# Performance work log

Hardware: AMD Instinct MI355X
Metric: run time of the kernel (lower is better)

## Reference

```python
import jax, jax.numpy as jnp
import numpy as np

B_, N_, D_ = 2, 2048, 512
E_ = 2 * D_          # d_inner = expand * dim
S_ = 16              # d_state
K_ = 4               # d_conv
R_ = 32              # dt_rank = ceil(dim/16)
C_ = 512             # cond_dim


def setup_inputs() -> dict:
    key = jax.random.key(0)
    ks = jax.random.split(key, 12)
    r = lambda i, sh, s=0.02: jax.random.normal(ks[i], sh, dtype=jnp.float32) * s
    return {
        "x": jax.random.normal(ks[0], (B_, N_, D_), dtype=jnp.float32),
        "cond": jax.random.normal(ks[1], (B_, C_), dtype=jnp.float32),
        "ln_g": jnp.ones((D_,), jnp.float32),
        "ln_b": jnp.zeros((D_,), jnp.float32),
        "W_in": r(2, (D_, 2 * E_)),            # in_proj (no bias)
        "conv_w": r(3, (E_, K_), 0.1),          # depthwise causal conv
        "conv_b": jnp.zeros((E_,), jnp.float32),
        "W_x": r(4, (E_, R_ + 2 * S_)),         # x_proj -> dt,B,C
        "W_dt": r(5, (R_, E_), 0.1),
        "b_dt": jnp.full((E_,), -4.6, jnp.float32),  # softplus(-4.6)~0.01
        "A_log": jnp.log(jnp.broadcast_to(jnp.arange(1, S_ + 1, dtype=jnp.float32), (E_, S_))),
        "D_skip": jnp.ones((E_,), jnp.float32),
        "W_out": r(6, (E_, D_)),                # out_proj (no bias)
        "film_gw": r(7, (C_, D_)),
        "film_gb": jnp.ones((D_,), jnp.float32),
        "film_bw": r(8, (C_, D_)),
        "film_bb": jnp.zeros((D_,), jnp.float32),
    }


def reference(x, cond, ln_g, ln_b, W_in, conv_w, conv_b, W_x, W_dt, b_dt,
              A_log, D_skip, W_out, film_gw, film_gb, film_bw, film_bb):
    # --- LayerNorm ---
    mu = x.mean(-1, keepdims=True)
    var = ((x - mu) ** 2).mean(-1, keepdims=True)
    xn = (x - mu) * jax.lax.rsqrt(var + 1e-5) * ln_g + ln_b

    # --- Mamba ---
    xz = xn @ W_in                                  # [B,N,2E]
    u, z = jnp.split(xz, 2, axis=-1)                # [B,N,E] each
    # causal depthwise conv1d (kernel K_), unrolled over small K
    up = jnp.pad(u, ((0, 0), (K_ - 1, 0), (0, 0)))
    uc = conv_b + sum(up[:, k:k + N_, :] * conv_w[:, k] for k in range(K_))
    uc = jax.nn.silu(uc)                            # [B,N,E]

    x_dbl = uc @ W_x                                # [B,N,R+2S]
    dt, Bm, Cm = jnp.split(x_dbl, [R_, R_ + S_], axis=-1)
    delta = jax.nn.softplus(dt @ W_dt + b_dt)       # [B,N,E]

    A = -jnp.exp(A_log)                             # [E,S]
    dA = jnp.exp(delta[..., None] * A)              # [B,N,E,S]
    dBu = (delta * uc)[..., None] * Bm[:, :, None, :]  # [B,N,E,S]

    def step(h, ins):
        dA_t, dBu_t, C_t = ins                      # [B,E,S],[B,E,S],[B,S]
        h = dA_t * h + dBu_t
        y = jnp.einsum('bes,bs->be', h, C_t)
        return h, y

    h0 = jnp.zeros((x.shape[0], E_, S_), dtype=x.dtype)
    _, ys = jax.lax.scan(step, h0,
                         (dA.swapaxes(0, 1), dBu.swapaxes(0, 1), Cm.swapaxes(0, 1)))
    y = ys.swapaxes(0, 1) + D_skip * uc             # [B,N,E]
    y = y * jax.nn.silu(z)
    out = y @ W_out                                 # [B,N,D]

    # --- FiLM ---
    gamma = cond @ film_gw + film_gb                # [B,D]
    beta = cond @ film_bw + film_bb
    return gamma[:, None, :] * out + beta[:, None, :]
```

## Files before the change

kernel.cpp:

```cpp
#include <hip/hip_runtime.h>
#include <hip/hip_bf16.h>
#include <math.h>

#define B_ 2
#define N_ 2048
#define D_ 512
#define E_ 1024
#define S_ 16
#define R_ 32
#define C_ 512
#define CH_ 32
#define NC_ (N_ / CH_)

using short8 = __attribute__((ext_vector_type(8))) short;
using f32x4  = __attribute__((ext_vector_type(4))) float;
using f32x16 = __attribute__((ext_vector_type(16))) float;

__device__ __forceinline__ short f2bf(float f) {
    union { float f; unsigned u; } x; x.f = f;
    unsigned r = (x.u + 0x7fffu + ((x.u >> 16) & 1u)) >> 16;
    return (short)r;
}
__device__ __forceinline__ float bf2f(short s) {
    union { unsigned u; float f; } x;
    x.u = ((unsigned)(unsigned short)s) << 16;
    return x.f;
}
__device__ __forceinline__ void gl_lds16(const void* g, void* l) {
    __builtin_amdgcn_global_load_lds((const __attribute__((address_space(1))) void*)g,
                                     (__attribute__((address_space(3))) void*)l, 16, 0, 0);
}

__global__ __launch_bounds__(256) void prep_kernel(
    const float* __restrict__ x, short* __restrict__ xnb,
    const float* __restrict__ W_in, short* __restrict__ Wint,
    const float* __restrict__ W_out, short* __restrict__ Woutt,
    const float* __restrict__ W_x, short* __restrict__ Wxt,
    const float* __restrict__ W_dt, short* __restrict__ Wdtt,
    const float* __restrict__ cond,
    const float* __restrict__ lng, const float* __restrict__ lnb,
    const float* __restrict__ gw, const float* __restrict__ gb,
    const float* __restrict__ bw, const float* __restrict__ bb,
    float* __restrict__ gamma, float* __restrict__ beta) {
    __shared__ __align__(16) float smem[2112];
    int bid = blockIdx.x;
    int tid = threadIdx.x;
    if (bid < 8) {
        float* cs = smem;
        float* red = smem + 1024;
        int d0 = bid * 64;
#pragma unroll
        for (int i = tid; i < 2 * C_ / 4; i += 256) {
            int b = i >> 7;
            int c4 = (i & 127) * 4;
            *(float4*)&cs[b * C_ + c4] = *(const float4*)(cond + (size_t)b * C_ + c4);
        }
        __syncthreads();
        int dl = tid & 63, ks = tid >> 6;
        int d = d0 + dl;
        float g0 = 0.f, g1 = 0.f, bt0 = 0.f, bt1 = 0.f;
#pragma unroll 4
        for (int k = ks * 128; k < ks * 128 + 128; k++) {
            float wg = gw[(size_t)k * D_ + d];
            float wb = bw[(size_t)k * D_ + d];
            float c0 = cs[k], c1 = cs[C_ + k];
            g0 = fmaf(c0, wg, g0);
            g1 = fmaf(c1, wg, g1);
            bt0 = fmaf(c0, wb, bt0);
            bt1 = fmaf(c1, wb, bt1);
        }
        red[(ks * 64 + dl) * 4 + 0] = g0; red[(ks * 64 + dl) * 4 + 1] = g1;
        red[(ks * 64 + dl) * 4 + 2] = bt0; red[(ks * 64 + dl) * 4 + 3] = bt1;
        __syncthreads();
        if (ks == 0) {
            float s0 = 0.f, s1 = 0.f, s2 = 0.f, s3 = 0.f;
#pragma unroll
            for (int q = 0; q < 4; q++) {
                s0 += red[(q * 64 + dl) * 4 + 0]; s1 += red[(q * 64 + dl) * 4 + 1];
                s2 += red[(q * 64 + dl) * 4 + 2]; s3 += red[(q * 64 + dl) * 4 + 3];
            }
            float gbv = gb[d], bbv = bb[d];
            gamma[d] = s0 + gbv;
            gamma[D_ + d] = s1 + gbv;
            beta[d] = s2 + bbv;
            beta[D_ + d] = s3 + bbv;
        }
    } else if (bid < 1640) {
        const float* W; short* Wt; int K, N, bx, by;
        int r = bid - 8;
        if (r < 1024)      { W = W_in;  Wt = Wint;  K = 512;  N = 2048; bx = r % 64; by = r / 64; }
        else if (r < 1536) { r -= 1024; W = W_out; Wt = Woutt; K = 1024; N = 512; bx = r % 16; by = r / 16; }
        else if (r < 1600) { r -= 1536; W = W_x;   Wt = Wxt;   K = 1024; N = 64;  bx = r % 2;  by = r / 2; }
        else               { r -= 1600; W = W_dt;  Wt = Wdtt;  K = 32;   N = 1024; bx = r;     by = 0; }
        float (*t)[33] = (float(*)[33])smem;
        int n0 = bx * 32, k0 = by * 32;
        int c = tid & 31, rr0 = tid >> 5;
#pragma unroll
        for (int rr = rr0; rr < 32; rr += 8)
            t[rr][c] = W[(size_t)(k0 + rr) * N + n0 + c];
        __syncthreads();
#pragma unroll
        for (int rr = rr0; rr < 32; rr += 8)
            Wt[(size_t)(n0 + rr) * K + k0 + c] = f2bf(t[c][rr]);
    } else {
        int t = bid - 1640;
        float2 v = *(const float2*)(x + (size_t)t * D_ + tid * 2);
        float s = v.x + v.y;
        float s2 = fmaf(v.x, v.x, v.y * v.y);
#pragma unroll
        for (int o = 32; o >= 1; o >>= 1) {
            s += __shfl_down(s, o);
            s2 += __shfl_down(s2, o);
        }
        int wid = tid >> 6;
        if ((tid & 63) == 0) { smem[wid] = s; smem[4 + wid] = s2; }
        __syncthreads();
        if (tid == 0) {
            float sum = smem[0] + smem[1] + smem[2] + smem[3];
            float sum2 = smem[4] + smem[5] + smem[6] + smem[7];
            float mu = sum * (1.f / (float)D_);
            float var = sum2 * (1.f / (float)D_) - mu * mu;
            smem[8] = mu;
            smem[9] = rsqrtf(var + 1e-5f);
        }
        __syncthreads();
        float mu = smem[8], rs = smem[9];
        float2 gv = *(const float2*)(lng + tid * 2);
        float2 bv = *(const float2*)(lnb + tid * 2);
        short2 o;
        o.x = f2bf((v.x - mu) * rs * gv.x + bv.x);
        o.y = f2bf((v.y - mu) * rs * gv.y + bv.y);
        *(short2*)(xnb + (size_t)t * D_ + tid * 2) = o;
    }
}

template <int BM, int BN, bool FILM, bool OBF>
__global__ __launch_bounds__(256) void gemm_bf16(
    const short* __restrict__ A, const short* __restrict__ Bt, void* __restrict__ Cv,
    int M, int N, int K,
    const float* __restrict__ gamma, const float* __restrict__ beta) {
    constexpr int BK = 64;
    constexpr int WM = BM / 2, WN = BN / 2;
    constexpr int MR = WM / 32, NR = WN / 32;
    __shared__ __align__(16) short As[BM * BK];
    __shared__ __align__(16) short Bs[BN * BK];
    int tid = threadIdx.x;
    int lane = tid & 63, w = tid >> 6;
    int wr = w >> 1, wc = w & 1;
    int lid = blockIdx.x;
    int chunk = gridDim.x >> 3;
    int swz = (lid & 7) * chunk + (lid >> 3);
    int ntiles = N / BN;
    int m0 = (swz / ntiles) * BM, n0 = (swz % ntiles) * BN;
    int lr = lane >> 3, lc = lane & 7;

    f32x16 acc[MR][NR];
#pragma unroll
    for (int i = 0; i < MR; i++)
#pragma unroll
        for (int j = 0; j < NR; j++)
#pragma unroll
            for (int r = 0; r < 16; r++) acc[i][j][r] = 0.f;

    int l31 = lane & 31, hk = (lane >> 5) * 8;

    for (int k0 = 0; k0 < K; k0 += BK) {
        __syncthreads();
#pragma unroll
        for (int ch = w; ch < BM / 8; ch += 4)
            gl_lds16(&A[(size_t)(m0 + ch * 8 + lr) * K + k0 + lc * 8], &As[ch * 512]);
#pragma unroll
        for (int ch = w; ch < BN / 8; ch += 4)
            gl_lds16(&Bt[(size_t)(n0 + ch * 8 + lr) * K + k0 + lc * 8], &Bs[ch * 512]);
        __syncthreads();
#pragma unroll
        for (int kk = 0; kk < 4; kk++) {
            short8 a[MR], b[NR];
#pragma unroll
            for (int i = 0; i < MR; i++)
                a[i] = *(const short8*)&As[(wr * WM + i * 32 + l31) * BK + kk * 16 + hk];
#pragma unroll
            for (int j = 0; j < NR; j++)
                b[j] = *(const short8*)&Bs[(wc * WN + j * 32 + l31) * BK + kk * 16 + hk];
#pragma unroll
            for (int i = 0; i < MR; i++)
#pragma unroll
                for (int j = 0; j < NR; j++)
                    acc[i][j] = __builtin_amdgcn_mfma_f32_32x32x16_bf16(a[i], b[j], acc[i][j], 0, 0, 0);
        }
    }
    int rbase = 4 * (lane >> 5);
    int bi = m0 >> 11;
#pragma unroll
    for (int i = 0; i < MR; i++)
#pragma unroll
        for (int j = 0; j < NR; j++) {
            int col = n0 + wc * WN + j * 32 + l31;
            float gm = 1.f, bt = 0.f;
            if (FILM) {
                gm = gamma[bi * D_ + col];
                bt = beta[bi * D_ + col];
            }
#pragma unroll
            for (int r = 0; r < 16; r++) {
                int row = m0 + wr * WM + i * 32 + rbase + (r & 3) + 8 * (r >> 2);
                float v = acc[i][j][r];
                if (FILM) v = gm * v + bt;
                if constexpr (OBF)
                    ((short*)Cv)[(size_t)row * N + col] = f2bf(v);
                else
                    ((float*)Cv)[(size_t)row * N + col] = v;
            }
        }
}

__global__ __launch_bounds__(512) void mid_kernel(
    const short* __restrict__ xzb, const float* __restrict__ cw, const float* __restrict__ cb,
    const short* __restrict__ Wxt,
    const short* __restrict__ Wdtt,
    const float* __restrict__ bdt,
    short* __restrict__ ucb, float* __restrict__ xdbl, short* __restrict__ deltab) {
    constexpr int LDU = 1032;
    __shared__ __align__(16) short u[16 * LDU];
    __shared__ __align__(16) float xd2[2][16 * 68];
    int tid = threadIdx.x;
    int t0 = blockIdx.x * 16;
    int n0 = t0 & (N_ - 1);
    {
        int c8 = (tid & 127) * 8;
        int base = (tid >> 7) * 4;
        float4 wv[8];
        float cbv[8];
#pragma unroll
        for (int j = 0; j < 8; j++) {
            wv[j] = *(const float4*)(cw + (c8 + j) * 4);
            cbv[j] = cb[c8 + j];
        }
        float uf[7][8];
#pragma unroll
        for (int j = 0; j < 7; j++) {
            short8 v = {0, 0, 0, 0, 0, 0, 0, 0};
            if (n0 + base - 3 + j >= 0)
                v = *(const short8*)&xzb[(size_t)(t0 + base - 3 + j) * (2 * E_) + c8];
#pragma unroll
            for (int q = 0; q < 8; q++) uf[j][q] = bf2f(v[q]);
        }
#pragma unroll
        for (int k = 0; k < 4; k++) {
            int n = base + k;
            short8 o;
#pragma unroll
            for (int q = 0; q < 8; q++) {
                float a = fmaf(wv[q].x, uf[k][q],
                          fmaf(wv[q].y, uf[k + 1][q],
                          fmaf(wv[q].z, uf[k + 2][q],
                          fmaf(wv[q].w, uf[k + 3][q], cbv[q]))));
                float v = a / (1.f + __expf(-a));
                o[q] = f2bf(v);
            }
            *(short8*)&ucb[(size_t)(t0 + n) * E_ + c8] = o;
            *(short8*)&u[n * LDU + c8] = o;
        }
    }
    __syncthreads();
    int lane = tid & 63, w = tid >> 6;
    int cg = w & 3, kh = w >> 2;
    int l15 = lane & 15, kq = (lane >> 4) * 8;
    f32x4 acc4 = {0.f, 0.f, 0.f, 0.f};
#pragma unroll 8
    for (int k0 = 0; k0 < 16; k0++) {
        int kk = kh * 512 + k0 * 32;
        short8 af = *(const short8*)&u[l15 * LDU + kk + kq];
        short8 bfr = *(const short8*)&Wxt[(size_t)(cg * 16 + l15) * E_ + kk + kq];
        acc4 = __builtin_amdgcn_mfma_f32_16x16x32_bf16(af, bfr, acc4, 0, 0, 0);
    }
#pragma unroll
    for (int j = 0; j < 4; j++)
        xd2[kh][((lane >> 4) * 4 + j) * 68 + cg * 16 + l15] = acc4[j];
    __syncthreads();
    if (tid < 256) {
        int r = tid >> 4, c4 = (tid & 15) * 4;
        float4 a = *(const float4*)&xd2[0][r * 68 + c4];
        float4 b = *(const float4*)&xd2[1][r * 68 + c4];
        a.x += b.x; a.y += b.y; a.z += b.z; a.w += b.w;
        *(float4*)&xd2[0][r * 68 + c4] = a;
        *(float4*)&xdbl[(size_t)(t0 + r) * 64 + c4] = a;
    }
    __syncthreads();
    float av[8];
    *(float4*)&av[0] = *(const float4*)&xd2[0][l15 * 68 + kq];
    *(float4*)&av[4] = *(const float4*)&xd2[0][l15 * 68 + kq + 4];
    short8 ab;
#pragma unroll
    for (int j = 0; j < 8; j++) ab[j] = f2bf(av[j]);
    int row4 = (lane >> 4) * 4;
#pragma unroll 4
    for (int t = 0; t < 8; t++) {
        int e = w * 128 + t * 16 + l15;
        short8 bb = *(const short8*)&Wdtt[(size_t)e * 32 + kq];
        f32x4 c4v = {0.f, 0.f, 0.f, 0.f};
        c4v = __builtin_amdgcn_mfma_f32_16x16x32_bf16(ab, bb, c4v, 0, 0, 0);
        float bv = bdt[e];
#pragma unroll
        for (int j = 0; j < 4; j++) {
            float xv = c4v[j] + bv;
            float sp = (xv > 20.f) ? xv : log1pf(__expf(xv));
            deltab[(size_t)(t0 + row4 + j) * E_ + e] = f2bf(sp);
        }
    }
}

__global__ __launch_bounds__(256) void scan_p1(const short* __restrict__ deltab,
                                               const short* __restrict__ ucb,
                                               const float* __restrict__ xdbl,
                                               const float* __restrict__ A_log,
                                               float* __restrict__ hend,
                                               float* __restrict__ cumd) {
    int blk = blockIdx.x;
    int eq = blk & 3;
    int c = (blk >> 2) & (NC_ - 1);
    int b = blk >> 8;
    int tid = threadIdx.x;
    int e = eq * 256 + tid;
    __shared__ float Bsl[CH_][16];
    int base = (b * N_ + c * CH_) * 64;
    for (int i = tid; i < CH_ * 16; i += 256) {
        int n = i >> 4, col = i & 15;
        Bsl[n][col] = xdbl[base + n * 64 + R_ + col];
    }
    float Aes[16];
    const float4* al = (const float4*)(A_log + e * 16);
#pragma unroll
    for (int j = 0; j < 4; j++) {
        float4 a = al[j];
        Aes[j * 4 + 0] = -__expf(a.x);
        Aes[j * 4 + 1] = -__expf(a.y);
        Aes[j * 4 + 2] = -__expf(a.z);
        Aes[j * 4 + 3] = -__expf(a.w);
    }
    __syncthreads();
    float h[16];
#pragma unroll
    for (int s = 0; s < 16; s++) h[s] = 0.f;
    float cum = 0.f;
    const short* dp = deltab + (size_t)(b * N_ + c * CH_) * E_ + e;
    const short* up = ucb + (size_t)(b * N_ + c * CH_) * E_ + e;
#pragma unroll 2
    for (int n = 0; n < CH_; n++) {
        float dv = bf2f(dp[n * E_]);
        float uv = bf2f(up[n * E_]);
        float du = dv * uv;
        cum += dv;
        float Bl[16];
#pragma unroll
        for (int j = 0; j < 4; j++) *(float4*)&Bl[j * 4] = *(const float4*)&Bsl[n][j * 4];
#pragma unroll
        for (int s = 0; s < 16; s++) {
            float dA = __expf(dv * Aes[s]);
            h[s] = fmaf(dA, h[s], du * Bl[s]);
        }
    }
    size_t ob = (size_t)(b * NC_ + c) * 16 * E_ + e;
#pragma unroll
    for (int s = 0; s < 16; s++) hend[ob + (size_t)s * E_] = h[s];
    cumd[(size_t)(b * NC_ + c) * E_ + e] = cum;
}

__global__ __launch_bounds__(256) void scan_comb(float* __restrict__ hend,
                                                 const float* __restrict__ cumd,
                                                 const float* __restrict__ A_log) {
    __shared__ float lh[64][65];
    __shared__ float lp[64][65];
    int blk = blockIdx.x;
    int et = blk & 15;
    int s = (blk >> 4) & 15;
    int b = blk >> 8;
    int e0 = et * 64;
    int tid = threadIdx.x;
    int lane = tid & 63, w = tid >> 6;
    for (int i = tid; i < 64 * 64; i += 256) {
        int c = i >> 6, e = i & 63;
        lh[c][e] = hend[((size_t)((b * NC_ + c) * 16) + s) * E_ + e0 + e];
        lp[c][e] = cumd[(size_t)(b * NC_ + c) * E_ + e0 + e];
    }
    __syncthreads();
#pragma unroll 4
    for (int q = 0; q < 16; q++) {
        int e = w * 16 + q;
        float Aes = -__expf(A_log[(e0 + e) * 16 + s]);
        float A = __expf(Aes * lp[lane][e]);
        float Bv = lh[lane][e];
#pragma unroll
        for (int off = 1; off < 64; off <<= 1) {
            float Ap = __shfl_up(A, off);
            float Bp = __shfl_up(Bv, off);
            if (lane >= off) {
                Bv = fmaf(A, Bp, Bv);
                A *= Ap;
            }
        }
        float hB = __shfl_up(Bv, 1);
        lh[lane][e] = (lane == 0) ? 0.f : hB;
    }
    __syncthreads();
    for (int i = tid; i < 64 * 64; i += 256) {
        int c = i >> 6, e = i & 63;
        hend[((size_t)((b * NC_ + c) * 16) + s) * E_ + e0 + e] = lh[c][e];
    }
}

__global__ __launch_bounds__(256) void scan_p3(const short* __restrict__ deltab,
                                               const short* __restrict__ ucb,
                                               const float* __restrict__ xdbl,
                                               const short* __restrict__ xzb,
                                               const float* __restrict__ A_log,
                                               const float* __restrict__ D_skip,
                                               const float* __restrict__ hend,
                                               short* __restrict__ yb) {
    int blk = blockIdx.x;
    int eq = blk & 3;
    int c = (blk >> 2) & (NC_ - 1);
    int b = blk >> 8;
    int tid = threadIdx.x;
    int e = eq * 256 + tid;
    __shared__ float Bsl[CH_][16];
    __shared__ float Csl[CH_][16];
    int base = (b * N_ + c * CH_) * 64;
    for (int i = tid; i < CH_ * 32; i += 256) {
        int n = i >> 5, col = i & 31;
        float v = xdbl[base + n * 64 + R_ + col];
        if (col < 16) Bsl[n][col] = v;
        else Csl[n][col - 16] = v;
    }
    float Aes[16];
    const float4* al = (const float4*)(A_log + e * 16);
#pragma unroll
    for (int j = 0; j < 4; j++) {
        float4 a = al[j];
        Aes[j * 4 + 0] = -__expf(a.x);
        Aes[j * 4 + 1] = -__expf(a.y);
        Aes[j * 4 + 2] = -__expf(a.z);
        Aes[j * 4 + 3] = -__expf(a.w);
    }
    float dsk = D_skip[e];
    float h[16];
    size_t ob = (size_t)(b * NC_ + c) * 16 * E_ + e;
#pragma unroll
    for (int s = 0; s < 16; s++) h[s] = hend[ob + (size_t)s * E_];
    __syncthreads();
    const short* dp = deltab + (size_t)(b * N_ + c * CH_) * E_ + e;
    const short* up = ucb + (size_t)(b * N_ + c * CH_) * E_ + e;
    const short* zp = xzb + (size_t)(b * N_ + c * CH_) * (2 * E_) + E_ + e;
    short* yp = yb + (size_t)(b * N_ + c * CH_) * E_ + e;
#pragma unroll 2
    for (int n = 0; n < CH_; n++) {
        float dv = bf2f(dp[n * E_]);
        float uv = bf2f(up[n * E_]);
        float du = dv * uv;
        float Bl[16], Cl[16];
#pragma unroll
        for (int j = 0; j < 4; j++) {
            *(float4*)&Bl[j * 4] = *(const float4*)&Bsl[n][j * 4];
            *(float4*)&Cl[j * 4] = *(const float4*)&Csl[n][j * 4];
        }
        float y = 0.f;
#pragma unroll
        for (int s = 0; s < 16; s++) {
            float dA = __expf(dv * Aes[s]);
            h[s] = fmaf(dA, h[s], du * Bl[s]);
            y = fmaf(h[s], Cl[s], y);
        }
        float zv = bf2f(zp[n * 2 * E_]);
        float yy = y + dsk * uv;
        yy = yy * (zv / (1.f + __expf(-zv)));
        yp[n * E_] = f2bf(yy);
    }
}

extern "C" void kernel_launch(void* const* d_in, const int* in_sizes, int n_in,
                              void* d_out, int out_size, void* d_ws, size_t ws_size,
                              hipStream_t stream) {
    const float* x       = (const float*)d_in[0];
    const float* cond    = (const float*)d_in[1];
    const float* ln_g    = (const float*)d_in[2];
    const float* ln_b    = (const float*)d_in[3];
    const float* W_in    = (const float*)d_in[4];
    const float* conv_w  = (const float*)d_in[5];
    const float* conv_b  = (const float*)d_in[6];
    const float* W_x     = (const float*)d_in[7];
    const float* W_dt    = (const float*)d_in[8];
    const float* b_dt    = (const float*)d_in[9];
    const float* A_log   = (const float*)d_in[10];
    const float* D_skip  = (const float*)d_in[11];
    const float* W_out   = (const float*)d_in[12];
    const float* film_gw = (const float*)d_in[13];
    const float* film_gb = (const float*)d_in[14];
    const float* film_bw = (const float*)d_in[15];
    const float* film_bb = (const float*)d_in[16];
    float* out = (float*)d_out;

    float* ws = (float*)d_ws;
    float* xdbl  = ws;
    float* gamma = xdbl + 262144;
    float* beta  = gamma + 1024;
    float* hend  = beta + 1024;
    float* cumd  = hend + 2097152;
    short* xzb   = (short*)(cumd + 131072);
    short* ucb   = xzb + 8388608;
    short* deltab = ucb + 4194304;
    short* Wint  = deltab + 4194304;
    short* Woutt = Wint + 1048576;
    short* yb    = Woutt + 524288;
    short* Wxt   = yb + 4194304;
    short* Wdtt  = Wxt + 65536;
    short* xnb   = Wdtt + 32768;

    prep_kernel<<<5736, 256, 0, stream>>>(
        x, xnb, W_in, Wint, W_out, Woutt, W_x, Wxt, W_dt, Wdtt,
        cond, ln_g, ln_b, film_gw, film_gb, film_bw, film_bb, gamma, beta);

    gemm_bf16<128, 128, false, true>
        <<<512, 256, 0, stream>>>(
            xnb, Wint, xzb, B_ * N_, 2 * E_, D_, nullptr, nullptr);

    mid_kernel<<<B_ * N_ / 16, 512, 0, stream>>>(
        xzb, conv_w, conv_b, Wxt, Wdtt, b_dt, ucb, xdbl, deltab);

    scan_p1<<<B_ * NC_ * 4, 256, 0, stream>>>(deltab, ucb, xdbl, A_log, hend, cumd);
    scan_comb<<<B_ * S_ * (E_ / 64), 256, 0, stream>>>(hend, cumd, A_log);
    scan_p3<<<B_ * NC_ * 4, 256, 0, stream>>>(deltab, ucb, xdbl, xzb, A_log, D_skip, hend, yb);

    gemm_bf16<64, 64, true, false>
        <<<512, 256, 0, stream>>>(
            yb, Woutt, out, B_ * N_, D_, E_, gamma, beta);
}
```

Measured before the change: 136.8 us.

## Overlap weight prep with first GEMM and store scan carry states in bf16

```diff
diff --git a/kernel.cpp b/kernel.cpp
--- a/kernel.cpp
+++ b/kernel.cpp
@@ -31,24 +31,136 @@
                                      (__attribute__((address_space(3))) void*)l, 16, 0, 0);
 }
 
-__global__ __launch_bounds__(256) void prep_kernel(
+__device__ __forceinline__ void transpose32(const float* __restrict__ W, short* __restrict__ Wt,
+                                            int K, int N, int bx, int by, float (*t)[33], int tid) {
+    int n0 = bx * 32, k0 = by * 32;
+    int c = tid & 31, rr0 = tid >> 5;
+#pragma unroll
+    for (int rr = rr0; rr < 32; rr += 8)
+        t[rr][c] = W[(size_t)(k0 + rr) * N + n0 + c];
+    __syncthreads();
+#pragma unroll
+    for (int rr = rr0; rr < 32; rr += 8)
+        Wt[(size_t)(n0 + rr) * K + k0 + c] = f2bf(t[c][rr]);
+}
+
+__global__ __launch_bounds__(256) void prep1_kernel(
     const float* __restrict__ x, short* __restrict__ xnb,
-    const float* __restrict__ W_in, short* __restrict__ Wint,
+    const float* __restrict__ lng, const float* __restrict__ lnb,
+    const float* __restrict__ W_in, short* __restrict__ Wint) {
+    __shared__ __align__(16) float smem[32 * 33];
+    int bid = blockIdx.x;
+    int tid = threadIdx.x;
+    if (bid < 1024) {
+        int t = bid * 4 + (tid >> 6);
+        int lane = tid & 63;
+        const float* src = x + (size_t)t * D_ + lane * 8;
+        float4 v0 = *(const float4*)src;
+        float4 v1 = *(const float4*)(src + 4);
+        float s = v0.x + v0.y + v0.z + v0.w + v1.x + v1.y + v1.z + v1.w;
+        float s2 = v0.x * v0.x;
+        s2 = fmaf(v0.y, v0.y, s2); s2 = fmaf(v0.z, v0.z, s2); s2 = fmaf(v0.w, v0.w, s2);
+        s2 = fmaf(v1.x, v1.x, s2); s2 = fmaf(v1.y, v1.y, s2);
+        s2 = fmaf(v1.z, v1.z, s2); s2 = fmaf(v1.w, v1.w, s2);
+#pragma unroll
+        for (int o = 32; o >= 1; o >>= 1) {
+            s += __shfl_xor(s, o);
+            s2 += __shfl_xor(s2, o);
+        }
+        float mu = s * (1.f / (float)D_);
+        float var = s2 * (1.f / (float)D_) - mu * mu;
+        float rs = rsqrtf(var + 1e-5f);
+        float4 g0 = *(const float4*)(lng + lane * 8);
+        float4 g1 = *(const float4*)(lng + lane * 8 + 4);
+        float4 b0 = *(const float4*)(lnb + lane * 8);
+        float4 b1 = *(const float4*)(lnb + lane * 8 + 4);
+        short8 o;
+        o[0] = f2bf((v0.x - mu) * rs * g0.x + b0.x);
+        o[1] = f2bf((v0.y - mu) * rs * g0.y + b0.y);
+        o[2] = f2bf((v0.z - mu) * rs * g0.z + b0.z);
+        o[3] = f2bf((v0.w - mu) * rs * g0.w + b0.w);
+        o[4] = f2bf((v1.x - mu) * rs * g1.x + b1.x);
+        o[5] = f2bf((v1.y - mu) * rs * g1.y + b1.y);
+        o[6] = f2bf((v1.z - mu) * rs * g1.z + b1.z);
+        o[7] = f2bf((v1.w - mu) * rs * g1.w + b1.w);
+        *(short8*)(xnb + (size_t)t * D_ + lane * 8) = o;
+    } else {
+        int r = bid - 1024;
+        transpose32(W_in, Wint, 512, 2048, r % 64, r / 64, (float(*)[33])smem, tid);
+    }
+}
+
+__global__ __launch_bounds__(256) void gemm1_hybrid(
+    const short* __restrict__ A, const short* __restrict__ Bt, short* __restrict__ Cb,
     const float* __restrict__ W_out, short* __restrict__ Woutt,
     const float* __restrict__ W_x, short* __restrict__ Wxt,
     const float* __restrict__ W_dt, short* __restrict__ Wdtt,
     const float* __restrict__ cond,
-    const float* __restrict__ lng, const float* __restrict__ lnb,
     const float* __restrict__ gw, const float* __restrict__ gb,
     const float* __restrict__ bw, const float* __restrict__ bb,
     float* __restrict__ gamma, float* __restrict__ beta) {
-    __shared__ __align__(16) float smem[2112];
+    __shared__ __align__(16) char smem[32768];
     int bid = blockIdx.x;
     int tid = threadIdx.x;
-    if (bid < 8) {
-        float* cs = smem;
-        float* red = smem + 1024;
-        int d0 = bid * 64;
+    if (bid < 512) {
+        constexpr int BM = 128, BN = 128, BK = 64;
+        constexpr int M = 4096, N = 2048, K = 512;
+        short* As = (short*)smem;
+        short* Bs = As + BM * BK;
+        int lane = tid & 63, w = tid >> 6;
+        int wr = w >> 1, wc = w & 1;
+        int swz = (bid & 7) * 64 + (bid >> 3);
+        int m0 = (swz >> 4) * BM, n0 = (swz & 15) * BN;
+        int lr = lane >> 3, lc = lane & 7;
+        f32x16 acc[2][2];
+#pragma unroll
+        for (int i = 0; i < 2; i++)
+#pragma unroll
+            for (int j = 0; j < 2; j++)
+#pragma unroll
+                for (int r = 0; r < 16; r++) acc[i][j][r] = 0.f;
+        int l31 = lane & 31, hk = (lane >> 5) * 8;
+        for (int k0 = 0; k0 < K; k0 += BK) {
+            __syncthreads();
+#pragma unroll
+            for (int ch = w; ch < BM / 8; ch += 4)
+                gl_lds16(&A[(size_t)(m0 + ch * 8 + lr) * K + k0 + lc * 8], &As[ch * 512]);
+#pragma unroll
+            for (int ch = w; ch < BN / 8; ch += 4)
+                gl_lds16(&Bt[(size_t)(n0 + ch * 8 + lr) * K + k0 + lc * 8], &Bs[ch * 512]);
+            __syncthreads();
+#pragma unroll
+            for (int kk = 0; kk < 4; kk++) {
+                short8 a[2], b[2];
+#pragma unroll
+                for (int i = 0; i < 2; i++)
+                    a[i] = *(const short8*)&As[(wr * 64 + i * 32 + l31) * BK + kk * 16 + hk];
+#pragma unroll
+                for (int j = 0; j < 2; j++)
+                    b[j] = *(const short8*)&Bs[(wc * 64 + j * 32 + l31) * BK + kk * 16 + hk];
+#pragma unroll
+                for (int i = 0; i < 2; i++)
+#pragma unroll
+                    for (int j = 0; j < 2; j++)
+                        acc[i][j] = __builtin_amdgcn_mfma_f32_32x32x16_bf16(a[i], b[j], acc[i][j], 0, 0, 0);
+            }
+        }
+        int rbase = 4 * (lane >> 5);
+#pragma unroll
+        for (int i = 0; i < 2; i++)
+#pragma unroll
+            for (int j = 0; j < 2; j++) {
+                int col = n0 + wc * 64 + j * 32 + l31;
+#pragma unroll
+                for (int r = 0; r < 16; r++) {
+                    int row = m0 + wr * 64 + i * 32 + rbase + (r & 3) + 8 * (r >> 2);
+                    Cb[(size_t)row * N + col] = f2bf(acc[i][j][r]);
+                }
+            }
+    } else if (bid < 520) {
+        float* cs = (float*)smem;
+        float* red = (float*)smem + 1024;
+        int d0 = (bid - 512) * 64;
 #pragma unroll
         for (int i = tid; i < 2 * C_ / 4; i += 256) {
             int b = i >> 7;
@@ -85,58 +197,21 @@
             beta[d] = s2 + bbv;
             beta[D_ + d] = s3 + bbv;
         }
-    } else if (bid < 1640) {
-        const float* W; short* Wt; int K, N, bx, by;
-        int r = bid - 8;
-        if (r < 1024)      { W = W_in;  Wt = Wint;  K = 512;  N = 2048; bx = r % 64; by = r / 64; }
-        else if (r < 1536) { r -= 1024; W = W_out; Wt = Woutt; K = 1024; N = 512; bx = r % 16; by = r / 16; }
-        else if (r < 1600) { r -= 1536; W = W_x;   Wt = Wxt;   K = 1024; N = 64;  bx = r % 2;  by = r / 2; }
-        else               { r -= 1600; W = W_dt;  Wt = Wdtt;  K = 32;   N = 1024; bx = r;     by = 0; }
-        float (*t)[33] = (float(*)[33])smem;
-        int n0 = bx * 32, k0 = by * 32;
-        int c = tid & 31, rr0 = tid >> 5;
-#pragma unroll
-        for (int rr = rr0; rr < 32; rr += 8)
-            t[rr][c] = W[(size_t)(k0 + rr) * N + n0 + c];
-        __syncthreads();
-#pragma unroll
-        for (int rr = rr0; rr < 32; rr += 8)
-            Wt[(size_t)(n0 + rr) * K + k0 + c] = f2bf(t[c][rr]);
+    } else if (bid < 1032) {
+        int r = bid - 520;
+        transpose32(W_out, Woutt, 1024, 512, r % 16, r / 16, (float(*)[33])smem, tid);
+    } else if (bid < 1096) {
+        int r = bid - 1032;
+        transpose32(W_x, Wxt, 1024, 64, r % 2, r / 2, (float(*)[33])smem, tid);
     } else {
-        int t = bid - 1640;
-        float2 v = *(const float2*)(x + (size_t)t * D_ + tid * 2);
-        float s = v.x + v.y;
-        float s2 = fmaf(v.x, v.x, v.y * v.y);
-#pragma unroll
-        for (int o = 32; o >= 1; o >>= 1) {
-            s += __shfl_down(s, o);
-            s2 += __shfl_down(s2, o);
-        }
-        int wid = tid >> 6;
-        if ((tid & 63) == 0) { smem[wid] = s; smem[4 + wid] = s2; }
-        __syncthreads();
-        if (tid == 0) {
-            float sum = smem[0] + smem[1] + smem[2] + smem[3];
-            float sum2 = smem[4] + smem[5] + smem[6] + smem[7];
-            float mu = sum * (1.f / (float)D_);
-            float var = sum2 * (1.f / (float)D_) - mu * mu;
-            smem[8] = mu;
-            smem[9] = rsqrtf(var + 1e-5f);
-        }
-        __syncthreads();
-        float mu = smem[8], rs = smem[9];
-        float2 gv = *(const float2*)(lng + tid * 2);
-        float2 bv = *(const float2*)(lnb + tid * 2);
-        short2 o;
-        o.x = f2bf((v.x - mu) * rs * gv.x + bv.x);
-        o.y = f2bf((v.y - mu) * rs * gv.y + bv.y);
-        *(short2*)(xnb + (size_t)t * D_ + tid * 2) = o;
-    }
-}
-
-template <int BM, int BN, bool FILM, bool OBF>
-__global__ __launch_bounds__(256) void gemm_bf16(
-    const short* __restrict__ A, const short* __restrict__ Bt, void* __restrict__ Cv,
+        int r = bid - 1096;
+        transpose32(W_dt, Wdtt, 32, 1024, r, 0, (float(*)[33])smem, tid);
+    }
+}
+
+template <int BM, int BN>
+__global__ __launch_bounds__(256) void gemm2_kernel(
+    const short* __restrict__ A, const short* __restrict__ Bt, float* __restrict__ Cf,
     int M, int N, int K,
     const float* __restrict__ gamma, const float* __restrict__ beta) {
     constexpr int BK = 64;
@@ -196,20 +271,12 @@
 #pragma unroll
         for (int j = 0; j < NR; j++) {
             int col = n0 + wc * WN + j * 32 + l31;
-            float gm = 1.f, bt = 0.f;
-            if (FILM) {
-                gm = gamma[bi * D_ + col];
-                bt = beta[bi * D_ + col];
-            }
+            float gm = gamma[bi * D_ + col];
+            float bt = beta[bi * D_ + col];
 #pragma unroll
             for (int r = 0; r < 16; r++) {
                 int row = m0 + wr * WM + i * 32 + rbase + (r & 3) + 8 * (r >> 2);
-                float v = acc[i][j][r];
-                if (FILM) v = gm * v + bt;
-                if constexpr (OBF)
-                    ((short*)Cv)[(size_t)row * N + col] = f2bf(v);
-                else
-                    ((float*)Cv)[(size_t)row * N + col] = v;
+                Cf[(size_t)row * N + col] = gm * acc[i][j][r] + bt;
             }
         }
 }
@@ -314,7 +381,7 @@
                                                const short* __restrict__ ucb,
                                                const float* __restrict__ xdbl,
                                                const float* __restrict__ A_log,
-                                               float* __restrict__ hend,
+                                               short* __restrict__ hend,
                                                float* __restrict__ cumd) {
     int blk = blockIdx.x;
     int eq = blk & 3;
@@ -362,11 +429,11 @@
     }
     size_t ob = (size_t)(b * NC_ + c) * 16 * E_ + e;
 #pragma unroll
-    for (int s = 0; s < 16; s++) hend[ob + (size_t)s * E_] = h[s];
+    for (int s = 0; s < 16; s++) hend[ob + (size_t)s * E_] = f2bf(h[s]);
     cumd[(size_t)(b * NC_ + c) * E_ + e] = cum;
 }
 
-__global__ __launch_bounds__(256) void scan_comb(float* __restrict__ hend,
+__global__ __launch_bounds__(256) void scan_comb(short* __restrict__ hend,
                                                  const float* __restrict__ cumd,
                                                  const float* __restrict__ A_log) {
     __shared__ float lh[64][65];
@@ -380,7 +447,7 @@
     int lane = tid & 63, w = tid >> 6;
     for (int i = tid; i < 64 * 64; i += 256) {
         int c = i >> 6, e = i & 63;
-        lh[c][e] = hend[((size_t)((b * NC_ + c) * 16) + s) * E_ + e0 + e];
+        lh[c][e] = bf2f(hend[((size_t)((b * NC_ + c) * 16) + s) * E_ + e0 + e]);
         lp[c][e] = cumd[(size_t)(b * NC_ + c) * E_ + e0 + e];
     }
     __syncthreads();
@@ -405,7 +472,7 @@
     __syncthreads();
     for (int i = tid; i < 64 * 64; i += 256) {
         int c = i >> 6, e = i & 63;
-        hend[((size_t)((b * NC_ + c) * 16) + s) * E_ + e0 + e] = lh[c][e];
+        hend[((size_t)((b * NC_ + c) * 16) + s) * E_ + e0 + e] = f2bf(lh[c][e]);
     }
 }
 
@@ -415,7 +482,7 @@
                                                const short* __restrict__ xzb,
                                                const float* __restrict__ A_log,
                                                const float* __restrict__ D_skip,
-                                               const float* __restrict__ hend,
+                                               const short* __restrict__ hend,
                                                short* __restrict__ yb) {
     int blk = blockIdx.x;
     int eq = blk & 3;
@@ -446,7 +513,7 @@
     float h[16];
     size_t ob = (size_t)(b * NC_ + c) * 16 * E_ + e;
 #pragma unroll
-    for (int s = 0; s < 16; s++) h[s] = hend[ob + (size_t)s * E_];
+    for (int s = 0; s < 16; s++) h[s] = bf2f(hend[ob + (size_t)s * E_]);
     __syncthreads();
     const short* dp = deltab + (size_t)(b * N_ + c * CH_) * E_ + e;
     const short* up = ucb + (size_t)(b * N_ + c * CH_) * E_ + e;
@@ -503,9 +570,9 @@
     float* xdbl  = ws;
     float* gamma = xdbl + 262144;
     float* beta  = gamma + 1024;
-    float* hend  = beta + 1024;
-    float* cumd  = hend + 2097152;
-    short* xzb   = (short*)(cumd + 131072);
+    float* cumd  = beta + 1024;
+    short* hend  = (short*)(cumd + 131072);
+    short* xzb   = hend + 2097152;
     short* ucb   = xzb + 8388608;
     short* deltab = ucb + 4194304;
     short* Wint  = deltab + 4194304;
@@ -515,13 +582,11 @@
     short* Wdtt  = Wxt + 65536;
     short* xnb   = Wdtt + 32768;
 
-    prep_kernel<<<5736, 256, 0, stream>>>(
-        x, xnb, W_in, Wint, W_out, Woutt, W_x, Wxt, W_dt, Wdtt,
-        cond, ln_g, ln_b, film_gw, film_gb, film_bw, film_bb, gamma, beta);
-
-    gemm_bf16<128, 128, false, true>
-        <<<512, 256, 0, stream>>>(
-            xnb, Wint, xzb, B_ * N_, 2 * E_, D_, nullptr, nullptr);
+    prep1_kernel<<<2048, 256, 0, stream>>>(x, xnb, ln_g, ln_b, W_in, Wint);
+
+    gemm1_hybrid<<<1128, 256, 0, stream>>>(
+        xnb, Wint, xzb, W_out, Woutt, W_x, Wxt, W_dt, Wdtt,
+        cond, film_gw, film_gb, film_bw, film_bb, gamma, beta);
 
     mid_kernel<<<B_ * N_ / 16, 512, 0, stream>>>(
         xzb, conv_w, conv_b, Wxt, Wdtt, b_dt, ucb, xdbl, deltab);
@@ -530,7 +595,7 @@
     scan_comb<<<B_ * S_ * (E_ / 64), 256, 0, stream>>>(hend, cumd, A_log);
     scan_p3<<<B_ * NC_ * 4, 256, 0, stream>>>(deltab, ucb, xdbl, xzb, A_log, D_skip, hend, yb);
 
-    gemm_bf16<64, 64, true, false>
+    gemm2_kernel<64, 64>
         <<<512, 256, 0, stream>>>(
             yb, Woutt, out, B_ * N_, D_, E_, gamma, beta);
 }
```

New measurement: 128.5 us. -6.1%, faster.
